# Optimization experiments

Measured on AMD Instinct MI355X. Metric: run time of the kernel, lower is better.

## Reference

```python
import jax, jax.numpy as jnp
import numpy as np

SCALES = (1, 2, 4)
KS = 5          # conv kernel size
POOL = 2        # maxpool kernel & stride


def coarse_grain(x, s):
    # non-overlapping mean pool along last axis
    B, C, L = x.shape
    Lc = L // s
    return x[:, :, : Lc * s].reshape(B, C, Lc, s).mean(axis=-1)


def conv1d(x, w, b):
    # x: [B, C_in, L], w: [C_out, C_in, K] (torch layout), VALID padding, stride 1
    y = jax.lax.conv_general_dilated(
        x, w, window_strides=(1,), padding='VALID',
        dimension_numbers=('NCH', 'OIH', 'NCH'))
    return y + b[None, :, None]


def maxpool1d(x, k):
    B, C, L = x.shape
    Lp = L // k
    return x[:, :, : Lp * k].reshape(B, C, Lp, k).max(axis=-1)


def conv_block(x, w1, b1, w2, b2):
    x = maxpool1d(jax.nn.relu(conv1d(x, w1, b1)), POOL)
    x = maxpool1d(jax.nn.relu(conv1d(x, w2, b2)), POOL)
    return x


def setup_inputs() -> dict:
    key = jax.random.key(0)
    ks = jax.random.split(key, 9)
    B, C, NWL = 2048, 4, 480
    C1, C2 = 16, 32
    # flatten size per model's own arithmetic: sum over scales of conv/pool output lens * C2
    F = (117 + 57 + 27) * C2  # 6432
    NOUT = 5
    sc = lambda fan_in: 1.0 / np.sqrt(fan_in)
    return {
        'x':  jax.random.normal(ks[0], (B, C, NWL), dtype=jnp.float32),
        'w1': jax.random.uniform(ks[1], (C1, C, KS), jnp.float32, -sc(C * KS), sc(C * KS)),
        'b1': jax.random.uniform(ks[2], (C1,), jnp.float32, -sc(C * KS), sc(C * KS)),
        'w2': jax.random.uniform(ks[3], (C2, C1, KS), jnp.float32, -sc(C1 * KS), sc(C1 * KS)),
        'b2': jax.random.uniform(ks[4], (C2,), jnp.float32, -sc(C1 * KS), sc(C1 * KS)),
        'wl': jax.random.uniform(ks[5], (F, F), jnp.float32, -sc(F), sc(F)),
        'bl': jax.random.uniform(ks[6], (F,), jnp.float32, -sc(F), sc(F)),
        'wo': jax.random.uniform(ks[7], (NOUT, F), jnp.float32, -sc(F), sc(F)),
        'bo': jax.random.uniform(ks[8], (NOUT,), jnp.float32, -sc(F), sc(F)),
    }


def reference(x, w1, b1, w2, b2, wl, bl, wo, bo):
    # multi-scale feature mapping: shared ConvBlock applied to each coarse-grained scale
    feats = [conv_block(coarse_grain(x, s), w1, b1, w2, b2) for s in SCALES]
    f = jnp.concatenate(feats, axis=-1)            # [B, 32, 201]
    f = f.reshape(f.shape[0], -1)                  # [B, 6432]
    # the SAME linear layer (shared weights) is applied 4 times in torch
    for _ in range(4):
        f = jax.nn.relu(f @ wl.T + bl)
    return f @ wo.T + bo                           # [B, 5]
```

## Files before the change

kernel.cpp:

```cpp
#include <hip/hip_runtime.h>

typedef _Float16 v8h __attribute__((ext_vector_type(8)));
typedef _Float16 v4h __attribute__((ext_vector_type(4)));
typedef float    v4f __attribute__((ext_vector_type(4)));

#define GK 6432
#define GN 6432
#define GM 2048
#define GNPAD 6528

__global__ void convert_w(const float* __restrict__ wl, _Float16* __restrict__ Wh)
{
    const int row = blockIdx.y;
    const int col = (blockIdx.x * 256 + threadIdx.x) * 4;
    if (col >= GK) return;
    v4h h;
    if (row < GN) {
        const float4 f = *(const float4*)(wl + (long)row * GK + col);
        h[0] = (_Float16)f.x; h[1] = (_Float16)f.y;
        h[2] = (_Float16)f.z; h[3] = (_Float16)f.w;
    } else {
        h[0] = (_Float16)0.f; h[1] = (_Float16)0.f;
        h[2] = (_Float16)0.f; h[3] = (_Float16)0.f;
    }
    *(v4h*)(Wh + (long)row * GK + col) = h;
}

#define SX   0
#define SX2  2048
#define SX4  3136
#define SW1  3712
#define SB1  4032
#define SW2  4048
#define SB2  6608
#define SP1  6640
#define LDSZ 13808

__global__ __launch_bounds__(256) void conv_feat(
    const float* __restrict__ x,
    const float* __restrict__ w1, const float* __restrict__ b1,
    const float* __restrict__ w2, const float* __restrict__ b2,
    _Float16* __restrict__ F0)
{
    __shared__ float lds[LDSZ];
    const int tid = threadIdx.x;
    const long b  = blockIdx.x;

    for (int i = tid; i < 1920; i += 256) {
        int c = i / 480, t = i % 480;
        lds[SX + c * 512 + t] = x[(b * 4 + c) * 480 + t];
    }
    for (int i = tid; i < 320;  i += 256) lds[SW1 + i] = w1[i];
    for (int i = tid; i < 16;   i += 256) lds[SB1 + i] = b1[i];
    for (int i = tid; i < 2560; i += 256) lds[SW2 + i] = w2[i];
    for (int i = tid; i < 32;   i += 256) lds[SB2 + i] = b2[i];
    __syncthreads();

    for (int i = tid; i < 960; i += 256) {
        int c = i / 240, t = i % 240;
        lds[SX2 + c * 272 + t] = 0.5f * (lds[SX + c * 512 + 2 * t] + lds[SX + c * 512 + 2 * t + 1]);
    }
    for (int i = tid; i < 480; i += 256) {
        int c = i / 120, t = i % 120;
        float s = lds[SX + c * 512 + 4 * t]     + lds[SX + c * 512 + 4 * t + 1]
                + lds[SX + c * 512 + 4 * t + 2] + lds[SX + c * 512 + 4 * t + 3];
        lds[SX4 + c * 144 + t] = 0.25f * s;
    }
    __syncthreads();

    for (int jid = tid; jid < 16 * 34; jid += 256) {
        const int c1 = jid / 34, rid = jid % 34;
        const int sidx = (rid < 19) ? 0 : (rid < 29 ? 1 : 2);
        const int r0   = (sidx == 0) ? rid : (sidx == 1 ? rid - 19 : rid - 29);
        const int u0   = r0 * 13;
        const int xbase  = (sidx == 0) ? SX  : (sidx == 1 ? SX2 : SX4);
        const int xpitch = (sidx == 0) ? 512 : (sidx == 1 ? 272 : 144);
        const int P      = (sidx == 0) ? 238 : (sidx == 1 ? 118 : 58);
        const int pofs   = (sidx == 0) ? 0   : (sidx == 1 ? 238 : 356);

        float acc[26];
        const float bias = lds[SB1 + c1];
        #pragma unroll
        for (int i = 0; i < 26; ++i) acc[i] = bias;

        #pragma unroll
        for (int ci = 0; ci < 4; ++ci) {
            float w[30];
            const float* xr = &lds[xbase + ci * xpitch + 2 * u0];
            #pragma unroll
            for (int q = 0; q < 15; ++q) {
                float2 t2 = *(const float2*)(xr + 2 * q);
                w[2 * q] = t2.x; w[2 * q + 1] = t2.y;
            }
            float wt[5];
            #pragma unroll
            for (int k = 0; k < 5; ++k) wt[k] = lds[SW1 + (c1 * 4 + ci) * 5 + k];
            #pragma unroll
            for (int i = 0; i < 26; ++i) {
                #pragma unroll
                for (int k = 0; k < 5; ++k) acc[i] += w[i + k] * wt[k];
            }
        }
        #pragma unroll
        for (int i = 0; i < 13; ++i) {
            int u = u0 + i;
            if (u < P)
                lds[SP1 + c1 * 448 + pofs + u] = fmaxf(fmaxf(acc[2 * i], acc[2 * i + 1]), 0.f);
        }
    }
    __syncthreads();

    for (int jid = tid; jid < 32 * 17; jid += 256) {
        const int c2 = jid / 17, rid = jid % 17;
        const int sidx = (rid < 9) ? 0 : (rid < 14 ? 1 : 2);
        const int r0   = (sidx == 0) ? rid : (sidx == 1 ? rid - 9 : rid - 14);
        const int v0   = r0 * 13;
        const int pbase = (sidx == 0) ? 0   : (sidx == 1 ? 238 : 356);
        const int Pv    = (sidx == 0) ? 117 : (sidx == 1 ? 57  : 27);
        const int vout  = (sidx == 0) ? 0   : (sidx == 1 ? 117 : 174);

        float acc[26];
        const float bias = lds[SB2 + c2];
        #pragma unroll
        for (int i = 0; i < 26; ++i) acc[i] = bias;

        for (int c1 = 0; c1 < 16; ++c1) {
            float w[30];
            const float* pr = &lds[SP1 + c1 * 448 + pbase + 2 * v0];
            #pragma unroll
            for (int q = 0; q < 15; ++q) {
                float2 t2 = *(const float2*)(pr + 2 * q);
                w[2 * q] = t2.x; w[2 * q + 1] = t2.y;
            }
            float wt[5];
            #pragma unroll
            for (int k = 0; k < 5; ++k) wt[k] = lds[SW2 + (c2 * 16 + c1) * 5 + k];
            #pragma unroll
            for (int i = 0; i < 26; ++i) {
                #pragma unroll
                for (int k = 0; k < 5; ++k) acc[i] += w[i + k] * wt[k];
            }
        }
        #pragma unroll
        for (int i = 0; i < 13; ++i) {
            int v = v0 + i;
            if (v < Pv) {
                float f = fmaxf(fmaxf(acc[2 * i], acc[2 * i + 1]), 0.f);
                F0[b * GK + c2 * 201 + vout + v] = (_Float16)f;
            }
        }
    }
}

__global__ __launch_bounds__(128, 2) void gemm_relu(
    const _Float16* __restrict__ A, const _Float16* __restrict__ Bw,
    const float* __restrict__ bias, _Float16* __restrict__ C)
{
    __shared__ _Float16 sA[2][128 * 32];
    __shared__ _Float16 sB[2][128 * 32];
    const int tid  = threadIdx.x;
    const int lane = tid & 63;
    const int wave = tid >> 6;

    const int id = blockIdx.x;
    int n_t, m_t;
    if (id < 768) {
        n_t = ((id >> 7) << 3) | (id & 7);
        m_t = (id >> 3) & 15;
    } else {
        const int r = id - 768;
        n_t = 48 + r % 3;
        m_t = r / 3;
    }
    const long tile_m = (long)m_t * 128;
    const long tile_n = (long)n_t * 128;

    const int lr   = lane >> 2;
    const int sfn  = (lr & 3) ^ ((lr >> 2) & 3);
    const int scol = (((lane & 3) ^ sfn) << 3);
    const _Float16* gS = (wave == 0)
        ? A  + (tile_m + lr) * (long)GK + scol
        : Bw + (tile_n + lr) * (long)GK + scol;

    const int fr = lane & 15;
    const int fp = lane >> 4;
    const int fslot = fp ^ ((fr & 3) ^ ((fr >> 2) & 3));
    int aoff[8], boff[4];
    #pragma unroll
    for (int i = 0; i < 8; ++i)
        aoff[i] = ((i << 4) + fr) * 32 + (fslot << 3);
    #pragma unroll
    for (int j = 0; j < 4; ++j)
        boff[j] = ((wave << 6) + (j << 4) + fr) * 32 + (fslot << 3);

    v4f acc[8][4];
    #pragma unroll
    for (int i = 0; i < 8; ++i) {
        #pragma unroll
        for (int j = 0; j < 4; ++j) { v4f z = {0.f, 0.f, 0.f, 0.f}; acc[i][j] = z; }
    }

    auto stage = [&](int k0, int buf) {
        _Float16* dst = (wave == 0) ? sA[buf] : sB[buf];
        #pragma unroll
        for (int t = 0; t < 8; ++t) {
            __builtin_amdgcn_global_load_lds(
                (const __attribute__((address_space(1))) void*)(gS + (t * 16) * (long)GK + k0),
                (__attribute__((address_space(3))) void*)(dst + t * 16 * 32), 16, 0, 0);
        }
    };

    stage(0, 0);
    int pb = 0;
    for (int k0 = 0; k0 < GK; k0 += 32) {
        __syncthreads();
        if (k0 + 32 < GK) stage(k0 + 32, pb ^ 1);

        const _Float16* cA = sA[pb];
        const _Float16* cB = sB[pb];
        v8h af[8], bf[4];
        #pragma unroll
        for (int j = 0; j < 4; ++j) bf[j] = *(const v8h*)&cB[boff[j]];
        #pragma unroll
        for (int i = 0; i < 8; ++i) af[i] = *(const v8h*)&cA[aoff[i]];
        #pragma unroll
        for (int i = 0; i < 8; ++i) {
            #pragma unroll
            for (int j = 0; j < 4; ++j)
                acc[i][j] = __builtin_amdgcn_mfma_f32_16x16x32_f16(af[i], bf[j], acc[i][j], 0, 0, 0);
        }
        pb ^= 1;
    }

    #pragma unroll
    for (int j = 0; j < 4; ++j) {
        const long col = tile_n + (wave << 6) + (j << 4) + fr;
        if (col < GN) {
            const float bv = bias[col];
            #pragma unroll
            for (int i = 0; i < 8; ++i) {
                const long row = tile_m + (i << 4) + (fp << 2);
                #pragma unroll
                for (int r = 0; r < 4; ++r) {
                    float v = acc[i][j][r] + bv;
                    v = v > 0.f ? v : 0.f;
                    C[(row + r) * (long)GN + col] = (_Float16)v;
                }
            }
        }
    }
}

__global__ __launch_bounds__(256) void final_out(
    const _Float16* __restrict__ F, const float* __restrict__ wo,
    const float* __restrict__ bo, float* __restrict__ out)
{
    __shared__ float red[4][8];
    const long b   = blockIdx.x;
    const int tid  = threadIdx.x;
    const int lane = tid & 63;
    const int wave = tid >> 6;
    float acc[5] = {0.f, 0.f, 0.f, 0.f, 0.f};
    const _Float16* f = F + b * GK;

    const int c1 = (wave + 1) * 402;
    for (int c = wave * 402 + lane; c < c1; c += 64) {
        const int k = c << 2;
        v4h f4 = *(const v4h*)(f + k);
        const float f0 = (float)f4[0], f1 = (float)f4[1];
        const float f2 = (float)f4[2], f3 = (float)f4[3];
        #pragma unroll
        for (int o = 0; o < 5; ++o) {
            const float4 w4 = *(const float4*)(wo + o * GK + k);
            acc[o] += f0 * w4.x + f1 * w4.y + f2 * w4.z + f3 * w4.w;
        }
    }
    #pragma unroll
    for (int o = 0; o < 5; ++o) {
        #pragma unroll
        for (int off = 32; off > 0; off >>= 1) acc[o] += __shfl_down(acc[o], off, 64);
    }
    if (lane == 0) {
        #pragma unroll
        for (int o = 0; o < 5; ++o) red[wave][o] = acc[o];
    }
    __syncthreads();
    if (tid < 5)
        out[b * 5 + tid] = red[0][tid] + red[1][tid] + red[2][tid] + red[3][tid] + bo[tid];
}

extern "C" void kernel_launch(void* const* d_in, const int* in_sizes, int n_in,
                              void* d_out, int out_size, void* d_ws, size_t ws_size,
                              hipStream_t stream)
{
    const float* x  = (const float*)d_in[0];
    const float* w1 = (const float*)d_in[1];
    const float* b1 = (const float*)d_in[2];
    const float* w2 = (const float*)d_in[3];
    const float* b2 = (const float*)d_in[4];
    const float* wl = (const float*)d_in[5];
    const float* bl = (const float*)d_in[6];
    const float* wo = (const float*)d_in[7];
    const float* bo = (const float*)d_in[8];
    float* out = (float*)d_out;

    char* ws = (char*)d_ws;
    _Float16* Wh = (_Float16*)ws;
    _Float16* F0 = (_Float16*)(ws + 83976192);
    _Float16* F1 = (_Float16*)(ws + 83976192 + 26345472);

    convert_w<<<dim3(7, GNPAD), 256, 0, stream>>>(wl, Wh);
    conv_feat<<<GM, 256, 0, stream>>>(x, w1, b1, w2, b2, F0);
    gemm_relu<<<816, 128, 0, stream>>>(F0, Wh, bl, F1);
    gemm_relu<<<816, 128, 0, stream>>>(F1, Wh, bl, F0);
    gemm_relu<<<816, 128, 0, stream>>>(F0, Wh, bl, F1);
    gemm_relu<<<816, 128, 0, stream>>>(F1, Wh, bl, F0);
    final_out<<<GM, 256, 0, stream>>>(F0, wo, bo, out);
}
```

Measured before the change: 1.350 ms.

## Replace GEMM with 256x256 eight-wave tiles and interleaved LDS staging schedule

Replaces the 128x128 four-wave-per-pair GEMM with a 256x256 tile, 512-thread kernel using K-step 64, padding K to 6528 so activations and weights have zero-padded rows. Global-to-LDS loads are interleaved with quarter-tile MFMA phases, using explicit barriers, waitcnts and setprio to overlap memory with compute. Larger tiles raise arithmetic intensity but give only 208 blocks on a GPU with 256 CUs, so some CUs sit idle. The explicit barriers may also add synchronisation cost.

```diff
diff --git a/kernel.cpp b/kernel.cpp
--- a/kernel.cpp
+++ b/kernel.cpp
@@ -7,15 +7,15 @@
 #define GK 6432
 #define GN 6432
 #define GM 2048
-#define GNPAD 6528
+#define KP 6528
 
 __global__ void convert_w(const float* __restrict__ wl, _Float16* __restrict__ Wh)
 {
     const int row = blockIdx.y;
     const int col = (blockIdx.x * 256 + threadIdx.x) * 4;
-    if (col >= GK) return;
+    if (col >= KP) return;
     v4h h;
-    if (row < GN) {
+    if (col < GK) {
         const float4 f = *(const float4*)(wl + (long)row * GK + col);
         h[0] = (_Float16)f.x; h[1] = (_Float16)f.y;
         h[2] = (_Float16)f.z; h[3] = (_Float16)f.w;
@@ -23,7 +23,7 @@
         h[0] = (_Float16)0.f; h[1] = (_Float16)0.f;
         h[2] = (_Float16)0.f; h[3] = (_Float16)0.f;
     }
-    *(v4h*)(Wh + (long)row * GK + col) = h;
+    *(v4h*)(Wh + (long)row * KP + col) = h;
 }
 
 #define SX   0
@@ -54,6 +54,7 @@
     for (int i = tid; i < 16;   i += 256) lds[SB1 + i] = b1[i];
     for (int i = tid; i < 2560; i += 256) lds[SW2 + i] = w2[i];
     for (int i = tid; i < 32;   i += 256) lds[SB2 + i] = b2[i];
+    for (int i = tid; i < KP - GK; i += 256) F0[b * KP + GK + i] = (_Float16)0.f;
     __syncthreads();
 
     for (int i = tid; i < 960; i += 256) {
@@ -146,53 +147,70 @@
             int v = v0 + i;
             if (v < Pv) {
                 float f = fmaxf(fmaxf(acc[2 * i], acc[2 * i + 1]), 0.f);
-                F0[b * GK + c2 * 201 + vout + v] = (_Float16)f;
-            }
-        }
-    }
-}
-
-__global__ __launch_bounds__(128, 2) void gemm_relu(
+                F0[b * KP + c2 * 201 + vout + v] = (_Float16)f;
+            }
+        }
+    }
+}
+
+__global__ __launch_bounds__(512, 2) void gemm8(
     const _Float16* __restrict__ A, const _Float16* __restrict__ Bw,
     const float* __restrict__ bias, _Float16* __restrict__ C)
 {
-    __shared__ _Float16 sA[2][128 * 32];
-    __shared__ _Float16 sB[2][128 * 32];
+    __shared__ _Float16 sA[2][256 * 64];
+    __shared__ _Float16 sB[2][256 * 64];
+
     const int tid  = threadIdx.x;
     const int lane = tid & 63;
     const int wave = tid >> 6;
-
-    const int id = blockIdx.x;
-    int n_t, m_t;
-    if (id < 768) {
-        n_t = ((id >> 7) << 3) | (id & 7);
-        m_t = (id >> 3) & 15;
-    } else {
-        const int r = id - 768;
-        n_t = 48 + r % 3;
-        m_t = r / 3;
-    }
-    const long tile_m = (long)m_t * 128;
-    const long tile_n = (long)n_t * 128;
-
-    const int lr   = lane >> 2;
-    const int sfn  = (lr & 3) ^ ((lr >> 2) & 3);
-    const int scol = (((lane & 3) ^ sfn) << 3);
-    const _Float16* gS = (wave == 0)
-        ? A  + (tile_m + lr) * (long)GK + scol
-        : Bw + (tile_n + lr) * (long)GK + scol;
+    const int wr   = wave >> 2;
+    const int wc   = wave & 3;
+
+    const int id  = blockIdx.x;
+    const long tile_m = (long)(id & 7) << 8;
+    const long tile_n = (long)(id >> 3) << 8;
+
+    const int lrow = lane >> 3;
+    const int lcol = ((lane & 7) ^ lrow) << 3;
+    const int rA1  = wave * 16 + ((wave & 4) << 4);
+    const int rA2  = rA1 + 64;
+    const int rB1  = wave * 16;
+    const int rB2  = rB1 + 128;
+
+    const _Float16* gA = A  + (tile_m + lrow) * (long)KP + lcol;
+    const _Float16* gB = Bw + lcol;
+
+#define STAGE_A(buf, row0, k0)                                                             \
+    {                                                                                      \
+        __builtin_amdgcn_global_load_lds(                                                  \
+            (const __attribute__((address_space(1))) void*)(gA + (long)(row0) * KP + (k0)),\
+            (__attribute__((address_space(3))) void*)(&sA[buf][(row0) * 64]), 16, 0, 0);   \
+        __builtin_amdgcn_global_load_lds(                                                  \
+            (const __attribute__((address_space(1))) void*)(gA + (long)((row0) + 8) * KP + (k0)), \
+            (__attribute__((address_space(3))) void*)(&sA[buf][((row0) + 8) * 64]), 16, 0, 0);    \
+    }
+
+#define STAGE_B(buf, row0, k0)                                                             \
+    {                                                                                      \
+        long r0_ = tile_n + (row0) + lrow;     if (r0_ > 6431) r0_ = 6431;                 \
+        long r1_ = r0_ + 8;                    if (r1_ > 6431) r1_ = 6431;                 \
+        __builtin_amdgcn_global_load_lds(                                                  \
+            (const __attribute__((address_space(1))) void*)(gB + r0_ * KP + (k0)),         \
+            (__attribute__((address_space(3))) void*)(&sB[buf][(row0) * 64]), 16, 0, 0);   \
+        __builtin_amdgcn_global_load_lds(                                                  \
+            (const __attribute__((address_space(1))) void*)(gB + r1_ * KP + (k0)),         \
+            (__attribute__((address_space(3))) void*)(&sB[buf][((row0) + 8) * 64]), 16, 0, 0);    \
+    }
 
     const int fr = lane & 15;
     const int fp = lane >> 4;
-    const int fslot = fp ^ ((fr & 3) ^ ((fr >> 2) & 3));
-    int aoff[8], boff[4];
-    #pragma unroll
-    for (int i = 0; i < 8; ++i)
-        aoff[i] = ((i << 4) + fr) * 32 + (fslot << 3);
-    #pragma unroll
-    for (int j = 0; j < 4; ++j)
-        boff[j] = ((wave << 6) + (j << 4) + fr) * 32 + (fslot << 3);
-
+    const int sw = fr & 7;
+    const int slot0 = (fp ^ sw) << 3;
+    const int slot1 = ((fp + 4) ^ sw) << 3;
+    const int abase = (wr * 128 + fr) * 64;
+    const int bbase = (wc * 64 + fr) * 64;
+
+    v8h af[4][2], bf0[2][2], bf1[2][2];
     v4f acc[8][4];
     #pragma unroll
     for (int i = 0; i < 8; ++i) {
@@ -200,55 +218,107 @@
         for (int j = 0; j < 4; ++j) { v4f z = {0.f, 0.f, 0.f, 0.f}; acc[i][j] = z; }
     }
 
-    auto stage = [&](int k0, int buf) {
-        _Float16* dst = (wave == 0) ? sA[buf] : sB[buf];
-        #pragma unroll
-        for (int t = 0; t < 8; ++t) {
-            __builtin_amdgcn_global_load_lds(
-                (const __attribute__((address_space(1))) void*)(gS + (t * 16) * (long)GK + k0),
-                (__attribute__((address_space(3))) void*)(dst + t * 16 * 32), 16, 0, 0);
-        }
-    };
-
-    stage(0, 0);
-    int pb = 0;
-    for (int k0 = 0; k0 < GK; k0 += 32) {
-        __syncthreads();
-        if (k0 + 32 < GK) stage(k0 + 32, pb ^ 1);
-
-        const _Float16* cA = sA[pb];
-        const _Float16* cB = sB[pb];
-        v8h af[8], bf[4];
-        #pragma unroll
-        for (int j = 0; j < 4; ++j) bf[j] = *(const v8h*)&cB[boff[j]];
-        #pragma unroll
-        for (int i = 0; i < 8; ++i) af[i] = *(const v8h*)&cA[aoff[i]];
-        #pragma unroll
-        for (int i = 0; i < 8; ++i) {
-            #pragma unroll
-            for (int j = 0; j < 4; ++j)
-                acc[i][j] = __builtin_amdgcn_mfma_f32_16x16x32_f16(af[i], bf[j], acc[i][j], 0, 0, 0);
-        }
-        pb ^= 1;
-    }
-
+#define LDA(base, h)                                                                       \
+    { _Pragma("unroll")                                                                    \
+      for (int mi = 0; mi < 4; ++mi) {                                                     \
+          af[mi][0] = *(const v8h*)((base) + abase + (h) * 4096 + mi * 1024 + slot0);      \
+          af[mi][1] = *(const v8h*)((base) + abase + (h) * 4096 + mi * 1024 + slot1);      \
+      } }
+
+#define LDB(base, h, bf)                                                                   \
+    { _Pragma("unroll")                                                                    \
+      for (int ni = 0; ni < 2; ++ni) {                                                     \
+          bf[ni][0] = *(const v8h*)((base) + bbase + (h) * 2048 + ni * 1024 + slot0);      \
+          bf[ni][1] = *(const v8h*)((base) + bbase + (h) * 2048 + ni * 1024 + slot1);      \
+      } }
+
+#define MMAQ(mh, nh, bf)                                                                   \
+    { _Pragma("unroll")                                                                    \
+      for (int mi = 0; mi < 4; ++mi) {                                                     \
+          _Pragma("unroll")                                                                \
+          for (int ni = 0; ni < 2; ++ni) {                                                 \
+              acc[(mh)*4+mi][(nh)*2+ni] = __builtin_amdgcn_mfma_f32_16x16x32_f16(          \
+                  af[mi][0], bf[ni][0], acc[(mh)*4+mi][(nh)*2+ni], 0, 0, 0);               \
+              acc[(mh)*4+mi][(nh)*2+ni] = __builtin_amdgcn_mfma_f32_16x16x32_f16(          \
+                  af[mi][1], bf[ni][1], acc[(mh)*4+mi][(nh)*2+ni], 0, 0, 0);               \
+          } } }
+
+    STAGE_A(0, rA1, 0);  STAGE_B(0, rB1, 0);  STAGE_A(0, rA2, 0);  STAGE_B(0, rB2, 0);
+    STAGE_A(1, rA1, 64); STAGE_B(1, rB1, 64); STAGE_A(1, rA2, 64);
+    asm volatile("s_waitcnt vmcnt(6)" ::: "memory");
+    __builtin_amdgcn_s_barrier();
+
+    int b = 0;
+    #pragma unroll 2
+    for (int kt = 0; kt < 102; ++kt, b ^= 1) {
+        const _Float16* cA = sA[b];
+        const _Float16* cB = sB[b];
+        const int k1 = (kt + 1) << 6;
+        const int k2 = (kt + 2) << 6;
+        const bool s1 = kt < 101;
+        const bool s2 = kt < 100;
+
+        LDA(cA, 0); LDB(cB, 0, bf0);
+        if (s1) STAGE_B(b ^ 1, rB2, k1);
+        __builtin_amdgcn_s_barrier();
+        asm volatile("s_waitcnt lgkmcnt(0)" ::: "memory");
+        __builtin_amdgcn_s_setprio(1);
+        MMAQ(0, 0, bf0);
+        __builtin_amdgcn_s_setprio(0);
+        __builtin_amdgcn_s_barrier();
+
+        LDB(cB, 1, bf1);
+        if (s2) STAGE_A(b, rA1, k2);
+        __builtin_amdgcn_s_barrier();
+        asm volatile("s_waitcnt lgkmcnt(0)" ::: "memory");
+        __builtin_amdgcn_s_setprio(1);
+        MMAQ(0, 1, bf1);
+        __builtin_amdgcn_s_setprio(0);
+        __builtin_amdgcn_s_barrier();
+
+        LDA(cA, 1);
+        if (s2) STAGE_B(b, rB1, k2);
+        __builtin_amdgcn_s_barrier();
+        asm volatile("s_waitcnt lgkmcnt(0)" ::: "memory");
+        __builtin_amdgcn_s_setprio(1);
+        MMAQ(1, 1, bf1);
+        __builtin_amdgcn_s_setprio(0);
+        __builtin_amdgcn_s_barrier();
+
+        if (s2) STAGE_A(b, rA2, k2);
+        __builtin_amdgcn_s_barrier();
+        __builtin_amdgcn_s_setprio(1);
+        MMAQ(1, 0, bf0);
+        __builtin_amdgcn_s_setprio(0);
+        if (s2) { asm volatile("s_waitcnt vmcnt(6)" ::: "memory"); }
+        else    { asm volatile("s_waitcnt vmcnt(0)" ::: "memory"); }
+        __builtin_amdgcn_s_barrier();
+    }
+
+    const long ccol0 = tile_n + wc * 64 + fr;
     #pragma unroll
-    for (int j = 0; j < 4; ++j) {
-        const long col = tile_n + (wave << 6) + (j << 4) + fr;
-        if (col < GN) {
-            const float bv = bias[col];
-            #pragma unroll
-            for (int i = 0; i < 8; ++i) {
-                const long row = tile_m + (i << 4) + (fp << 2);
+    for (int n = 0; n < 4; ++n) {
+        const long col = ccol0 + n * 16;
+        if (col < KP) {
+            const bool valid = col < GN;
+            const float bv = valid ? bias[col] : 0.f;
+            #pragma unroll
+            for (int m = 0; m < 8; ++m) {
+                const long row = tile_m + wr * 128 + m * 16 + fp * 4;
                 #pragma unroll
                 for (int r = 0; r < 4; ++r) {
-                    float v = acc[i][j][r] + bv;
+                    float v = acc[m][n][r] + bv;
                     v = v > 0.f ? v : 0.f;
-                    C[(row + r) * (long)GN + col] = (_Float16)v;
+                    C[(row + r) * (long)KP + col] = valid ? (_Float16)v : (_Float16)0.f;
                 }
             }
         }
     }
+#undef STAGE_A
+#undef STAGE_B
+#undef LDA
+#undef LDB
+#undef MMAQ
 }
 
 __global__ __launch_bounds__(256) void final_out(
@@ -261,7 +331,7 @@
     const int lane = tid & 63;
     const int wave = tid >> 6;
     float acc[5] = {0.f, 0.f, 0.f, 0.f, 0.f};
-    const _Float16* f = F + b * GK;
+    const _Float16* f = F + b * KP;
 
     const int c1 = (wave + 1) * 402;
     for (int c = wave * 402 + lane; c < c1; c += 64) {
@@ -307,13 +377,13 @@
     char* ws = (char*)d_ws;
     _Float16* Wh = (_Float16*)ws;
     _Float16* F0 = (_Float16*)(ws + 83976192);
-    _Float16* F1 = (_Float16*)(ws + 83976192 + 26345472);
-
-    convert_w<<<dim3(7, GNPAD), 256, 0, stream>>>(wl, Wh);
+    _Float16* F1 = (_Float16*)(ws + 83976192 + 26738688);
+
+    convert_w<<<dim3(7, GN), 256, 0, stream>>>(wl, Wh);
     conv_feat<<<GM, 256, 0, stream>>>(x, w1, b1, w2, b2, F0);
-    gemm_relu<<<816, 128, 0, stream>>>(F0, Wh, bl, F1);
-    gemm_relu<<<816, 128, 0, stream>>>(F1, Wh, bl, F0);
-    gemm_relu<<<816, 128, 0, stream>>>(F0, Wh, bl, F1);
-    gemm_relu<<<816, 128, 0, stream>>>(F1, Wh, bl, F0);
+    gemm8<<<208, 512, 0, stream>>>(F0, Wh, bl, F1);
+    gemm8<<<208, 512, 0, stream>>>(F1, Wh, bl, F0);
+    gemm8<<<208, 512, 0, stream>>>(F0, Wh, bl, F1);
+    gemm8<<<208, 512, 0, stream>>>(F1, Wh, bl, F0);
     final_out<<<GM, 256, 0, stream>>>(F0, wo, bo, out);
 }
```

Result: faster. 1.150 ms (-14.8%).
